# Kernel tuning notes

Measured on AMD Instinct MI355X. Metric: run time of the kernel, lower is better.

## Reference

```python
import jax, jax.numpy as jnp
import numpy as np

NUM_HEADS = 12
ALPHA = 4.0
EPS = 1e-6

def safe_pow(x, p):
    # relu(x)**p with grad-safe handling of x<=0 (avoids nan from log(0) in pow grads)
    xp = jnp.where(x > 0, x, 1.0)
    return jnp.where(x > 0, xp ** p, 0.0)

def setup_inputs() -> dict:
    key = jax.random.key(0)
    ks = jax.random.split(key, 9)
    B, N, C = 8, 4096, 768
    Hn, hd, ksz = NUM_HEADS, C // NUM_HEADS, 5
    return {
        "x": jax.random.normal(ks[0], (B, N, C), jnp.float32),
        "Wqg": jax.random.normal(ks[1], (C, 2 * C), jnp.float32) * 0.02,
        "Wkv": jax.random.normal(ks[2], (C, 2 * C), jnp.float32) * 0.02,
        "Wproj": jax.random.normal(ks[3], (C, C), jnp.float32) * 0.02,
        "bproj": jnp.zeros((C,), jnp.float32),
        "dwc_w": jax.random.normal(ks[4], (hd, 1, ksz, ksz), jnp.float32) * 0.05,
        "dwc_b": jnp.zeros((hd,), jnp.float32),
        "power_p": jax.random.normal(ks[5], (1, Hn, 1, hd), jnp.float32) * 0.01,
        "scale_p": jax.random.normal(ks[6], (1, 1, C), jnp.float32) * 0.01,
        "pos_enc": jax.random.normal(ks[7], (1, N, C), jnp.float32) * 0.01,
    }

def reference(x, Wqg, Wkv, Wproj, bproj, dwc_w, dwc_b, power_p, scale_p, pos_enc):
    B, N, C = x.shape
    Hn = NUM_HEADS
    hd = C // Hn
    # q/g projection: [B,N,2C] -> q = [...,0,:], g = [...,1,:]
    qg = (x @ Wqg).reshape(B, N, 2, C)
    q, g = qg[:, :, 0], qg[:, :, 1]
    # k/v projection (sr_ratio == 1)
    kvp = x @ Wkv
    k, v = kvp[..., :C], kvp[..., C:]
    k = k + pos_enc
    scale = jax.nn.softplus(scale_p)            # [1,1,C]
    power = 1.0 + ALPHA * jax.nn.sigmoid(power_p)  # [1,Hn,1,hd]
    q = q / scale
    k = k / scale
    # -> [B,Hn,N,hd]
    q = q.reshape(B, N, Hn, hd).transpose(0, 2, 1, 3)
    k = k.reshape(B, N, Hn, hd).transpose(0, 2, 1, 3)
    v = v.reshape(B, N, Hn, hd).transpose(0, 2, 1, 3)
    q_pos = safe_pow(q, power)
    q_neg = safe_pow(-q, power)
    k_pos = safe_pow(k, power)
    k_neg = safe_pow(-k, power)
    q_sim = jnp.concatenate([q_pos, q_neg], -1)  # [B,Hn,N,2hd]
    q_opp = jnp.concatenate([q_neg, q_pos], -1)
    k_cat = jnp.concatenate([k_pos, k_neg], -1)
    v1, v2 = jnp.split(v, 2, axis=-1)            # [B,Hn,N,hd/2]
    n = N
    inv_n = 1.0 / n
    k_mean = k_cat.mean(axis=2, keepdims=True)   # [B,Hn,1,2hd]
    z_sim = 1.0 / (jnp.einsum('bhnk,bhmk->bhnm', q_sim, k_mean) + EPS)  # [B,Hn,N,1]
    kv1 = jnp.einsum('bhnk,bhnv->bhkv', k_cat, v1) * inv_n
    x_sim = jnp.einsum('bhnk,bhkv->bhnv', q_sim, kv1) * z_sim
    z_opp = 1.0 / (jnp.einsum('bhnk,bhmk->bhnm', q_opp, k_mean) + EPS)
    kv2 = jnp.einsum('bhnk,bhnv->bhkv', k_cat, v2) * inv_n
    x_opp = jnp.einsum('bhnk,bhkv->bhnv', q_opp, kv2) * z_opp
    xa = jnp.concatenate([x_sim, x_opp], -1).transpose(0, 2, 1, 3).reshape(B, N, C)
    # depthwise-conv positional branch on v (head-major channel layout)
    Hs = int(np.sqrt(N))
    v_img = v.reshape(B * Hn, Hs, Hs, hd).transpose(0, 3, 1, 2)  # [B*Hn, hd, Hs, Hs]
    v_conv = jax.lax.conv_general_dilated(
        v_img, dwc_w, (1, 1), 'SAME', feature_group_count=hd,
        dimension_numbers=('NCHW', 'OIHW', 'NCHW')) + dwc_b[None, :, None, None]
    v_pos = v_conv.reshape(B, C, N).transpose(0, 2, 1)  # [B,N,C]
    out = (xa + v_pos) * g
    return out @ Wproj + bproj
```

## Files before the change

### kernel.cpp

```cpp
#include <hip/hip_runtime.h>


typedef _Float16 f16;
typedef __attribute__((ext_vector_type(4))) float f32x4;
typedef __attribute__((ext_vector_type(8))) _Float16 f16x8;
typedef __attribute__((ext_vector_type(4))) _Float16 f16x4;

__device__ __forceinline__ void mfma(f32x4& c, f16x8 a, f16x8 b) {
  c = __builtin_amdgcn_mfma_f32_16x16x32_f16(a, b, c, 0, 0, 0);
}

__device__ __forceinline__ void gload_lds16(const f16* g, f16* l) {
  __builtin_amdgcn_global_load_lds(
      (__attribute__((address_space(1))) void*)g,
      (__attribute__((address_space(3))) void*)l, 16, 0, 0);
}

__device__ __forceinline__ f16x8 relu8(f16x8 v) {
  f16x8 r;
#pragma unroll
  for (int u = 0; u < 8; ++u) r[u] = (v[u] > (f16)0) ? v[u] : (f16)0;
  return r;
}
__device__ __forceinline__ f16x8 nrelu8(f16x8 v) {
  f16x8 r;
#pragma unroll
  for (int u = 0; u < 8; ++u) r[u] = (v[u] < (f16)0) ? (f16)(-v[u]) : (f16)0;
  return r;
}

__global__ void prep_scalars_kernel(const float* __restrict__ scale_p,
                                    const float* __restrict__ power_p,
                                    float* __restrict__ iscale,
                                    float* __restrict__ powr) {
  int c = blockIdx.x * 256 + threadIdx.x;
  if (c < 768) {
    float sp = scale_p[c];
    float s = (sp > 20.f) ? sp : log1pf(__expf(sp));
    iscale[c] = 1.f / s;
    powr[c] = 1.f + 4.f / (1.f + __expf(-power_p[c]));
  }
}

__global__ __launch_bounds__(256) void cast_x_kernel(const float* __restrict__ x,
                                                     f16* __restrict__ xblk) {
  __shared__ f16 tile[128 * 72];
  const int kb = blockIdx.x, mt = blockIdx.y, t = threadIdx.x;
  const float* xp = x + (size_t)mt * 128 * 768 + kb * 64;
#pragma unroll
  for (int it = 0; it < 8; ++it) {
    int idx = it * 256 + t;
    int row = idx >> 4, kc4 = (idx & 15) * 4;
    f32x4 v = *(const f32x4*)(xp + (size_t)row * 768 + kc4);
    f16x4 h;
    h[0] = (f16)v[0]; h[1] = (f16)v[1]; h[2] = (f16)v[2]; h[3] = (f16)v[3];
    *(f16x4*)(tile + row * 72 + kc4) = h;
  }
  __syncthreads();
  f16* op = xblk + (size_t)mt * 98304 + kb * 8192;
#pragma unroll
  for (int it = 0; it < 4; ++it) {
    int c = it * 256 + t;
    int kchunk = c >> 7, m = c & 127;
    f16x4 lo = *(const f16x4*)(tile + m * 72 + kchunk * 8);
    f16x4 hi = *(const f16x4*)(tile + m * 72 + kchunk * 8 + 4);
    *(f16x4*)(op + c * 8) = lo;
    *(f16x4*)(op + c * 8 + 4) = hi;
  }
}

__global__ __launch_bounds__(256) void transpose_w_kernel(const float* __restrict__ W,
                                                          f16* __restrict__ outblk,
                                                          int Cc, int col_off) {
  __shared__ float tile[32][33];
  const int c0 = blockIdx.x * 32, r0 = blockIdx.y * 32, t = threadIdx.x;
#pragma unroll
  for (int it = 0; it < 4; ++it) {
    int rr = it * 8 + (t >> 5), cc = t & 31;
    tile[rr][cc] = W[(size_t)(r0 + rr) * Cc + c0 + cc];
  }
  __syncthreads();
  if (t < 128) {
    int cl = t >> 2, rb = t & 3;
    int cg = col_off + c0 + cl;
    int rg = r0 + rb * 8;
    f16x4 v0, v1;
#pragma unroll
    for (int u = 0; u < 4; ++u) v0[u] = (f16)tile[rb * 8 + u][cl];
#pragma unroll
    for (int u = 0; u < 4; ++u) v1[u] = (f16)tile[rb * 8 + 4 + u][cl];
    size_t base = (size_t)(cg >> 7) * 98304 + (size_t)(rg >> 3) * 1024 +
                  (size_t)(cg & 127) * 8;
    *(f16x4*)(outblk + base) = v0;
    *(f16x4*)(outblk + base + 4) = v1;
  }
}

template <int MODE>
__global__ __launch_bounds__(512, 4) void gemm_kernel(
    const f16* __restrict__ Ablk, const f16* __restrict__ Bblk,
    const float* __restrict__ powr, const float* __restrict__ iscale,
    const float* __restrict__ pos_enc, const float* __restrict__ bproj,
    f16* __restrict__ qpow, f16* __restrict__ gbuf, f16* __restrict__ kpow,
    f16* __restrict__ vt, float* __restrict__ outp) {
  constexpr int A_SZ = 4096;
  constexpr int STR  = 12288;
  __shared__ f16 smem[2 * STR];
  const int t = threadIdx.x;
  const int wid = t >> 6, lane = t & 63;
  const int c16 = lane & 15, q = lane >> 4;
  const int ntile = blockIdx.x, mtile = blockIdx.y;
  const int wm = wid >> 2, wn = wid & 3;
  const int bh2 = wn >> 1, bc = (wn & 1) * 64;
  const f16* Ap = Ablk + (size_t)mtile * 98304;
  const f16* Bp = Bblk + (size_t)ntile * 196608;

  auto STAGE = [&](int buf, int k0) {
    const size_t gk = (size_t)(k0 >> 3) * 1024;
    gload_lds16(Ap + gk + (size_t)t * 8, smem + buf * STR + wid * 512);
    gload_lds16(Bp + gk + (size_t)t * 8, smem + buf * STR + A_SZ + wid * 512);
    gload_lds16(Bp + 98304 + gk + (size_t)t * 8,
                smem + buf * STR + A_SZ + 4096 + wid * 512);
  };

  f32x4 acc[4][4];
#pragma unroll
  for (int i = 0; i < 4; ++i)
#pragma unroll
    for (int j = 0; j < 4; ++j) acc[i][j] = (f32x4){0.f, 0.f, 0.f, 0.f};

  STAGE(0, 0);
  asm volatile("s_waitcnt vmcnt(0)");
  __builtin_amdgcn_sched_barrier(0);
  __builtin_amdgcn_s_barrier();
  __builtin_amdgcn_sched_barrier(0);

  for (int j = 0; j < 24; ++j) {
    const int cur = j & 1;
    if (j < 23) STAGE(cur ^ 1, (j + 1) * 32);
    const f16* A_ = smem + cur * STR;
    const f16* B_ = smem + cur * STR + A_SZ + bh2 * 4096;
    f16x8 af[4], bf[4];
    const int kc = q * 1024;
#pragma unroll
    for (int mi = 0; mi < 4; ++mi)
      af[mi] = *(const f16x8*)(A_ + kc + (wm * 64 + mi * 16 + c16) * 8);
#pragma unroll
    for (int ni = 0; ni < 4; ++ni)
      bf[ni] = *(const f16x8*)(B_ + kc + (bc + ni * 16 + c16) * 8);
    asm volatile("s_waitcnt lgkmcnt(0)");
    __builtin_amdgcn_sched_barrier(0);
    __builtin_amdgcn_s_setprio(1);
#pragma unroll
    for (int mi = 0; mi < 4; ++mi)
#pragma unroll
      for (int ni = 0; ni < 4; ++ni) mfma(acc[mi][ni], af[mi], bf[ni]);
    __builtin_amdgcn_s_setprio(0);
    __builtin_amdgcn_sched_barrier(0);
    if (j < 23) asm volatile("s_waitcnt vmcnt(0)");
    __builtin_amdgcn_sched_barrier(0);
    __builtin_amdgcn_s_barrier();
    __builtin_amdgcn_sched_barrier(0);
  }

  if (MODE == 0) {
    const int sec = ntile / 3;
    const int csb = (ntile - sec * 3) * 256;
    const int b = mtile >> 5;
    const int nim0 = (mtile & 31) * 128;
#pragma unroll
    for (int mi = 0; mi < 4; ++mi) {
      const int nloc = nim0 + wm * 64 + mi * 16 + q * 4;
#pragma unroll
      for (int ni = 0; ni < 4; ++ni) {
        const int cs = csb + wn * 64 + ni * 16 + c16;
        const int h = cs >> 6, d = cs & 63;
        const int bh = b * 12 + h;
        if (sec == 0) {
          const float p = powr[cs], isc = iscale[cs];
          const size_t qb2 = (size_t)bh * 262144 + (size_t)(nloc >> 7) * 8192;
          const int dpo = (d >> 3) * 1024 + (d & 7);
#pragma unroll
          for (int r2 = 0; r2 < 4; ++r2) {
            float val = acc[mi][ni][r2] * isc;
            float av = fabsf(val);
            float e = (av > 0.f) ? exp2f(p * __log2f(av)) : 0.f;
            float s = (val > 0.f) ? e : ((val < 0.f) ? -e : 0.f);
            int mrow = (nloc + r2) & 127;
            qpow[qb2 + mrow * 8 + dpo] = (f16)s;
          }
        } else if (sec == 1) {
#pragma unroll
          for (int r2 = 0; r2 < 4; ++r2)
            gbuf[((size_t)bh * 4096 + nloc + r2) * 64 + d] = (f16)acc[mi][ni][r2];
        } else if (sec == 2) {
          const float p = powr[cs], isc = iscale[cs];
          f16x4 pk;
#pragma unroll
          for (int r2 = 0; r2 < 4; ++r2) {
            int n = nloc + r2;
            float val = (acc[mi][ni][r2] + pos_enc[(size_t)n * 768 + cs]) * isc;
            float av = fabsf(val);
            float e = (av > 0.f) ? exp2f(p * __log2f(av)) : 0.f;
            pk[r2] = (f16)((val > 0.f) ? e : ((val < 0.f) ? -e : 0.f));
          }
          const size_t kb2 =
              (size_t)bh * 262144 + (size_t)(nloc >> 3) * 512 + (nloc & 7);
          *(f16x4*)(kpow + kb2 + (size_t)d * 8) = pk;
        } else {
          f16x4 vv4;
#pragma unroll
          for (int r2 = 0; r2 < 4; ++r2) vv4[r2] = (f16)acc[mi][ni][r2];
          *(f16x4*)(vt + (size_t)(bh * 64 + d) * 4096 + nloc) = vv4;
        }
      }
    }
  } else {
#pragma unroll
    for (int mi = 0; mi < 4; ++mi) {
      const int tok0 = mtile * 128 + wm * 64 + mi * 16 + q * 4;
#pragma unroll
      for (int ni = 0; ni < 4; ++ni) {
        const int col = ntile * 256 + wn * 64 + ni * 16 + c16;
        const float bb = bproj[col];
#pragma unroll
        for (int r2 = 0; r2 < 4; ++r2)
          outp[(size_t)(tok0 + r2) * 768 + col] = acc[mi][ni][r2] + bb;
      }
    }
  }
}

__global__ __launch_bounds__(256) void kv_kernel(const f16* __restrict__ kpow,
                                                 const f16* __restrict__ vt,
                                                 float* __restrict__ kvp,
                                                 float* __restrict__ ksp) {
  __shared__ f16 Ks[8192];
  __shared__ f16 Vs[4096];
  __shared__ float rp[256], rn[256];
  const int bh = blockIdx.x, split = blockIdx.y, t = threadIdx.x;
  const int wave = t >> 6, lane = t & 63;
  const int c16 = lane & 15, q = lane >> 4;
  const f16* kb = kpow + (size_t)bh * 262144;
  const f16* vb = vt + (size_t)bh * 64 * 4096;
  f32x4 acc[4][2];
#pragma unroll
  for (int i = 0; i < 4; ++i)
#pragma unroll
    for (int j = 0; j < 2; ++j) acc[i][j] = (f32x4){0.f, 0.f, 0.f, 0.f};
  float sp = 0.f, sn = 0.f;

  const int n_beg = split * 1024, n_end = n_beg + 1024;
  for (int n0 = n_beg; n0 < n_end; n0 += 64) {
    f16x8 kr[2], vr[2];
#pragma unroll
    for (int r = 0; r < 2; ++r)
      kr[r] = *(const f16x8*)(kb + (size_t)n0 * 64 + (size_t)(r * 256 + t) * 8);
#pragma unroll
    for (int r = 0; r < 2; ++r) {
      int cc = r * 256 + t;
      int vv = cc >> 3, nc = cc & 7;
      vr[r] = *(const f16x8*)(vb + (size_t)vv * 4096 + n0 + nc * 8);
    }
#pragma unroll
    for (int r = 0; r < 2; ++r)
#pragma unroll
      for (int u = 0; u < 8; ++u) {
        float f = (float)kr[r][u];
        sp += (f > 0.f) ? f : 0.f;
        sn += (f < 0.f) ? -f : 0.f;
      }
    __syncthreads();
#pragma unroll
    for (int r = 0; r < 2; ++r) {
      int cp = r * 256 + t;
      int nch = cp >> 6, d = cp & 63;
      *(f16x8*)(Ks + (size_t)(nch * 1024 + d * 8)) = relu8(kr[r]);
      *(f16x8*)(Ks + (size_t)(nch * 1024 + (d + 64) * 8)) = nrelu8(kr[r]);
    }
#pragma unroll
    for (int r = 0; r < 2; ++r) {
      int cc = r * 256 + t;
      int vv = cc >> 3, nc = cc & 7;
      *(f16x8*)(Vs + (size_t)(nc * 64 + (vv ^ nc)) * 8) = vr[r];
    }
    __syncthreads();
#pragma unroll
    for (int s = 0; s < 2; ++s) {
      f16x8 af[4], bf2[2];
#pragma unroll
      for (int i = 0; i < 4; ++i) {
        int m = i * 16 + c16, nc2 = s * 4 + q;
        af[i] = *(const f16x8*)(Vs + (nc2 * 64 + (m ^ nc2)) * 8);
      }
#pragma unroll
      for (int j = 0; j < 2; ++j)
        bf2[j] = *(const f16x8*)(Ks + ((s * 4 + q) * 128 + wave * 32 + j * 16 + c16) * 8);
#pragma unroll
      for (int i = 0; i < 4; ++i)
#pragma unroll
        for (int j = 0; j < 2; ++j) mfma(acc[i][j], af[i], bf2[j]);
    }
    __syncthreads();
  }
  float* kvb = kvp + (size_t)(bh * 4 + split) * 8192;
#pragma unroll
  for (int i = 0; i < 4; ++i)
#pragma unroll
    for (int j = 0; j < 2; ++j) {
      int kk = wave * 32 + j * 16 + c16;
      int vv0 = i * 16 + q * 4;
#pragma unroll
      for (int r2 = 0; r2 < 4; ++r2)
        kvb[(size_t)(vv0 + r2) * 128 + kk] = acc[i][j][r2];
    }
  rp[t] = sp; rn[t] = sn;
  __syncthreads();
  if (t < 64) {
    float* ko = ksp + (size_t)(bh * 4 + split) * 128;
    ko[t] = rp[t] + rp[t + 64] + rp[t + 128] + rp[t + 192];
    ko[64 + t] = rn[t] + rn[t + 64] + rn[t + 128] + rn[t + 192];
  }
}

__global__ void bx_kernel(const float* __restrict__ kvp,
                          const float* __restrict__ ksp, f16* __restrict__ bxt) {
  const int bh = blockIdx.x, kk = threadIdx.x;
  const float inv_n = 1.f / 4096.f;
  const float* kv0 = kvp + (size_t)bh * 4 * 8192;
  const float* ks0 = ksp + (size_t)bh * 4 * 128;
  f16* ob = bxt + (size_t)bh * 80 * 128;
  for (int nn = 0; nn < 32; ++nn) {
    float v = kv0[nn * 128 + kk] + kv0[8192 + nn * 128 + kk] +
              kv0[16384 + nn * 128 + kk] + kv0[24576 + nn * 128 + kk];
    ob[nn * 128 + kk] = (f16)(v * inv_n);
  }
  const int kx = kk ^ 64;
  for (int nn = 32; nn < 64; ++nn) {
    float v = kv0[nn * 128 + kx] + kv0[8192 + nn * 128 + kx] +
              kv0[16384 + nn * 128 + kx] + kv0[24576 + nn * 128 + kx];
    ob[nn * 128 + kk] = (f16)(v * inv_n);
  }
  float s0 = ks0[kk] + ks0[128 + kk] + ks0[256 + kk] + ks0[384 + kk];
  ob[64 * 128 + kk] = (f16)(s0 * inv_n);
  float s1 = ks0[kx] + ks0[128 + kx] + ks0[256 + kx] + ks0[384 + kx];
  ob[65 * 128 + kk] = (f16)(s1 * inv_n);
  for (int nn = 66; nn < 80; ++nn) ob[nn * 128 + kk] = (f16)0.f;
}

__global__ __launch_bounds__(256) void conv_kernel(const f16* __restrict__ vt,
                                                   const float* __restrict__ w,
                                                   const float* __restrict__ bias,
                                                   f16* __restrict__ vpos) {
  __shared__ float img[68 * 69];
  const int blk = blockIdx.x;
  const int d = blk & 63, bh = blk >> 6;
  const f16* src = vt + (size_t)(bh * 64 + d) * 4096;
  for (int i = threadIdx.x; i < 68 * 68; i += 256) {
    int yy = i / 68, xx = i - yy * 68;
    int y = yy - 2, x = xx - 2;
    float val = 0.f;
    if (((unsigned)y < 64u) && ((unsigned)x < 64u)) val = (float)src[y * 64 + x];
    img[yy * 69 + xx] = val;
  }
  float wr[25];
#pragma unroll
  for (int k = 0; k < 25; ++k) wr[k] = w[d * 25 + k];
  const float bb = bias[d];
  __syncthreads();
  f16* dst = vpos + (size_t)(bh * 64 + d) * 4096;
  for (int g4 = threadIdx.x; g4 < 1024; g4 += 256) {
    int y = g4 >> 4, x4 = (g4 & 15) * 4;
    float o0 = bb, o1 = bb, o2 = bb, o3 = bb;
#pragma unroll
    for (int ky = 0; ky < 5; ++ky) {
      const float* row = img + (y + ky) * 69 + x4;
      float r[8];
#pragma unroll
      for (int u = 0; u < 8; ++u) r[u] = row[u];
#pragma unroll
      for (int kx = 0; kx < 5; ++kx) {
        float wv = wr[ky * 5 + kx];
        o0 += r[kx] * wv;
        o1 += r[kx + 1] * wv;
        o2 += r[kx + 2] * wv;
        o3 += r[kx + 3] * wv;
      }
    }
    f16x4 st;
    st[0] = (f16)o0; st[1] = (f16)o1; st[2] = (f16)o2; st[3] = (f16)o3;
    *(f16x4*)(dst + y * 64 + x4) = st;
  }
}

__global__ __launch_bounds__(256) void xa_kernel(
    const f16* __restrict__ qpow, const f16* __restrict__ bxt,
    const f16* __restrict__ vpos, const f16* __restrict__ gbuf,
    f16* __restrict__ pre) {
  __shared__ f16 Qs[16384];
  __shared__ f16 Ps[64 * 134];
  __shared__ float zs[256];
  const int nb = blockIdx.x, bh = blockIdx.y;
  const int b = bh / 12, h = bh % 12;
  const int t = threadIdx.x;
  const int wave = t >> 6, lane = t & 63;
  const int c16 = lane & 15, q = lane >> 4;
  const f16* qb = qpow + (size_t)bh * 262144 + (size_t)nb * 8192;
  f16x8 qr[4];
#pragma unroll
  for (int r = 0; r < 4; ++r)
    qr[r] = *(const f16x8*)(qb + (size_t)(r * 256 + t) * 8);
#pragma unroll
  for (int r = 0; r < 4; ++r) {
    int c = r * 256 + t;
    int dch = c >> 7, row = c & 127;
    *(f16x8*)(Qs + (size_t)(dch * 1024 + row * 8)) = relu8(qr[r]);
    *(f16x8*)(Qs + (size_t)((dch + 8) * 1024 + row * 8)) = nrelu8(qr[r]);
  }
  {
    const f16* vpb = vpos + (size_t)bh * 262144 + (size_t)nb * 128;
#pragma unroll
    for (int it = 0; it < 4; ++it) {
      int idx = it * 256 + t;
      int col = idx >> 4, nc = idx & 15;
      f16x8 v = *(const f16x8*)(vpb + (size_t)col * 4096 + nc * 8);
      *(f16x8*)(Ps + col * 134 + nc * 8) = v;
    }
  }
  __syncthreads();
  f32x4 acc[2][5];
#pragma unroll
  for (int i = 0; i < 2; ++i)
#pragma unroll
    for (int j = 0; j < 5; ++j) acc[i][j] = (f32x4){0.f, 0.f, 0.f, 0.f};
  const f16* bx = bxt + (size_t)bh * 80 * 128;
#pragma unroll
  for (int s = 0; s < 4; ++s) {
    f16x8 af[2], bf5[5];
#pragma unroll
    for (int i = 0; i < 2; ++i)
      af[i] = *(const f16x8*)(Qs + ((s * 4 + q) * 1024 + (wave * 32 + i * 16 + c16) * 8));
#pragma unroll
    for (int j = 0; j < 5; ++j)
      bf5[j] = *(const f16x8*)(bx + (size_t)(j * 16 + c16) * 128 + s * 32 + q * 8);
#pragma unroll
    for (int i = 0; i < 2; ++i)
#pragma unroll
      for (int j = 0; j < 5; ++j) mfma(acc[i][j], af[i], bf5[j]);
  }
  if (c16 < 2) {
#pragma unroll
    for (int i = 0; i < 2; ++i) {
      int mloc = wave * 32 + i * 16 + q * 4;
#pragma unroll
      for (int r2 = 0; r2 < 4; ++r2) zs[(mloc + r2) * 2 + c16] = acc[i][4][r2];
    }
  }
  __syncthreads();
#pragma unroll
  for (int i = 0; i < 2; ++i) {
    const int mbase = wave * 32 + i * 16 + q * 4;
#pragma unroll
    for (int j = 0; j < 4; ++j) {
      const int col = j * 16 + c16;
      const int cch = h * 64 + col;
      const int zsel = col >> 5;
#pragma unroll
      for (int r2 = 0; r2 < 4; ++r2) {
        const int mloc = mbase + r2;
        const int n = nb * 128 + mloc;
        const float den = zs[mloc * 2 + zsel];
        const float xav = acc[i][j][r2] / (den + 1e-6f);
        const float vp = (float)Ps[col * 134 + mloc];
        const float gg = (float)gbuf[((size_t)bh * 4096 + n) * 64 + col];
        const int tok = b * 4096 + n;
        pre[(size_t)(tok >> 7) * 98304 + (size_t)(cch >> 3) * 1024 +
            (tok & 127) * 8 + (cch & 7)] = (f16)((xav + vp) * gg);
      }
    }
  }
}

extern "C" void kernel_launch(void* const* d_in, const int* in_sizes, int n_in,
                              void* d_out, int out_size, void* d_ws, size_t ws_size,
                              hipStream_t stream) {
  const float* x       = (const float*)d_in[0];
  const float* Wqg     = (const float*)d_in[1];
  const float* Wkv     = (const float*)d_in[2];
  const float* Wproj   = (const float*)d_in[3];
  const float* bproj   = (const float*)d_in[4];
  const float* dwc_w   = (const float*)d_in[5];
  const float* dwc_b   = (const float*)d_in[6];
  const float* power_p = (const float*)d_in[7];
  const float* scale_p = (const float*)d_in[8];
  const float* pos_enc = (const float*)d_in[9];
  float* outp = (float*)d_out;

  char* ws = (char*)d_ws;
  constexpr size_t o_qpow = 0;
  constexpr size_t o_kpow = 50331648;
  constexpr size_t o_vt   = 100663296;
  constexpr size_t o_gbuf = 150994944;
  constexpr size_t o_xblk = 201326592;
  constexpr size_t o_wta  = 251658240;
  constexpr size_t o_wtp  = 256376832;
  constexpr size_t o_isc  = 257556480;
  constexpr size_t o_pwr  = 257560576;
  constexpr size_t o_bxt  = 257564672;

  f16*   qpow = (f16*)(ws + o_qpow);
  f16*   kpow = (f16*)(ws + o_kpow);
  f16*   vt   = (f16*)(ws + o_vt);
  f16*   gbuf = (f16*)(ws + o_gbuf);
  f16*   xblk = (f16*)(ws + o_xblk);
  f16*   wta  = (f16*)(ws + o_wta);
  f16*   wtp  = (f16*)(ws + o_wtp);
  float* isc  = (float*)(ws + o_isc);
  float* pwr  = (float*)(ws + o_pwr);
  f16*   bxt  = (f16*)(ws + o_bxt);
  float* kvp  = (float*)(ws + o_xblk);
  float* ksp  = (float*)(ws + o_xblk + 12582912);
  f16*   vpos = kpow;
  f16*   pre  = xblk;

  prep_scalars_kernel<<<dim3(3), 256, 0, stream>>>(scale_p, power_p, isc, pwr);
  cast_x_kernel<<<dim3(12, 256), 256, 0, stream>>>(x, xblk);
  transpose_w_kernel<<<dim3(48, 24), 256, 0, stream>>>(Wqg, wta, 1536, 0);
  transpose_w_kernel<<<dim3(48, 24), 256, 0, stream>>>(Wkv, wta, 1536, 1536);
  transpose_w_kernel<<<dim3(24, 24), 256, 0, stream>>>(Wproj, wtp, 768, 0);
  gemm_kernel<0><<<dim3(12, 256), 512, 0, stream>>>(
      xblk, wta, pwr, isc, pos_enc, nullptr, qpow, gbuf, kpow, vt, nullptr);
  kv_kernel<<<dim3(96, 4), 256, 0, stream>>>(kpow, vt, kvp, ksp);
  bx_kernel<<<96, 128, 0, stream>>>(kvp, ksp, bxt);
  conv_kernel<<<6144, 256, 0, stream>>>(vt, dwc_w, dwc_b, vpos);
  xa_kernel<<<dim3(32, 96), 256, 0, stream>>>(qpow, bxt, vpos, gbuf, pre);
  gemm_kernel<1><<<dim3(3, 256), 512, 0, stream>>>(
      pre, wtp, nullptr, nullptr, nullptr, bproj, nullptr, nullptr, nullptr,
      nullptr, outp);
}
```

Measured before the change: 617.0 us.

## Triple-buffer GEMM staging, block gbuf layout, vectorize conv and xa global I/O

The GEMM main loop moves from two to three LDS stages and prefetches two k-steps ahead, waiting only on the older stage's loads. The g projection is now written in the same blocked token/channel layout as the pre-projection buffer. The xa kernel can then load g with coalesced 16-byte reads, stage its output tile in LDS and write it back with vector stores instead of scattered 2-byte writes. The conv kernel loads its image rows as 4-wide f16 vectors and zeroes the halo columns separately. The extra GEMM stage raises LDS use per block, which may lower occupancy at the 4-blocks-per-CU launch bound.

```diff
diff --git a/kernel.cpp b/kernel.cpp
--- a/kernel.cpp
+++ b/kernel.cpp
@@ -105,7 +105,7 @@
     f16* __restrict__ vt, float* __restrict__ outp) {
   constexpr int A_SZ = 4096;
   constexpr int STR  = 12288;
-  __shared__ f16 smem[2 * STR];
+  __shared__ f16 smem[3 * STR];
   const int t = threadIdx.x;
   const int wid = t >> 6, lane = t & 63;
   const int c16 = lane & 15, q = lane >> 4;
@@ -130,14 +130,15 @@
     for (int j = 0; j < 4; ++j) acc[i][j] = (f32x4){0.f, 0.f, 0.f, 0.f};
 
   STAGE(0, 0);
-  asm volatile("s_waitcnt vmcnt(0)");
+  STAGE(1, 32);
+  asm volatile("s_waitcnt vmcnt(3)");
   __builtin_amdgcn_sched_barrier(0);
   __builtin_amdgcn_s_barrier();
   __builtin_amdgcn_sched_barrier(0);
 
+  int cur = 0, nx2 = 2;
   for (int j = 0; j < 24; ++j) {
-    const int cur = j & 1;
-    if (j < 23) STAGE(cur ^ 1, (j + 1) * 32);
+    if (j < 22) STAGE(nx2, (j + 2) * 32);
     const f16* A_ = smem + cur * STR;
     const f16* B_ = smem + cur * STR + A_SZ + bh2 * 4096;
     f16x8 af[4], bf[4];
@@ -157,10 +158,13 @@
       for (int ni = 0; ni < 4; ++ni) mfma(acc[mi][ni], af[mi], bf[ni]);
     __builtin_amdgcn_s_setprio(0);
     __builtin_amdgcn_sched_barrier(0);
-    if (j < 23) asm volatile("s_waitcnt vmcnt(0)");
+    if (j < 22)       asm volatile("s_waitcnt vmcnt(3)");
+    else if (j == 22) asm volatile("s_waitcnt vmcnt(0)");
     __builtin_amdgcn_sched_barrier(0);
     __builtin_amdgcn_s_barrier();
     __builtin_amdgcn_sched_barrier(0);
+    cur = (cur == 2) ? 0 : cur + 1;
+    nx2 = (nx2 == 2) ? 0 : nx2 + 1;
   }
 
   if (MODE == 0) {
@@ -191,8 +195,11 @@
           }
         } else if (sec == 1) {
 #pragma unroll
-          for (int r2 = 0; r2 < 4; ++r2)
-            gbuf[((size_t)bh * 4096 + nloc + r2) * 64 + d] = (f16)acc[mi][ni][r2];
+          for (int r2 = 0; r2 < 4; ++r2) {
+            const int tok = b * 4096 + nloc + r2;
+            gbuf[(size_t)(tok >> 7) * 98304 + (size_t)(cs >> 3) * 1024 +
+                 (tok & 127) * 8 + (cs & 7)] = (f16)acc[mi][ni][r2];
+          }
         } else if (sec == 2) {
           const float p = powr[cs], isc = iscale[cs];
           f16x4 pk;
@@ -356,12 +363,21 @@
   const int blk = blockIdx.x;
   const int d = blk & 63, bh = blk >> 6;
   const f16* src = vt + (size_t)(bh * 64 + d) * 4096;
-  for (int i = threadIdx.x; i < 68 * 68; i += 256) {
-    int yy = i / 68, xx = i - yy * 68;
-    int y = yy - 2, x = xx - 2;
-    float val = 0.f;
-    if (((unsigned)y < 64u) && ((unsigned)x < 64u)) val = (float)src[y * 64 + x];
-    img[yy * 69 + xx] = val;
+  for (int i = threadIdx.x; i < 68 * 16; i += 256) {
+    int yy = i >> 4, g4 = i & 15;
+    int y = yy - 2;
+    float v0 = 0.f, v1 = 0.f, v2 = 0.f, v3 = 0.f;
+    if ((unsigned)y < 64u) {
+      f16x4 v = *(const f16x4*)(src + y * 64 + g4 * 4);
+      v0 = (float)v[0]; v1 = (float)v[1]; v2 = (float)v[2]; v3 = (float)v[3];
+    }
+    float* row = img + yy * 69 + 2 + g4 * 4;
+    row[0] = v0; row[1] = v1; row[2] = v2; row[3] = v3;
+  }
+  for (int i = threadIdx.x; i < 68 * 4; i += 256) {
+    int yy = i >> 2, c = i & 3;
+    int xx = (c < 2) ? c : 64 + c;
+    img[yy * 69 + xx] = 0.f;
   }
   float wr[25];
 #pragma unroll
@@ -406,10 +422,14 @@
   const int wave = t >> 6, lane = t & 63;
   const int c16 = lane & 15, q = lane >> 4;
   const f16* qb = qpow + (size_t)bh * 262144 + (size_t)nb * 8192;
-  f16x8 qr[4];
+  const size_t gp2 = (size_t)(b * 32 + nb) * 98304 + (size_t)(h * 8) * 1024;
+  f16x8 qr[4], gr[4];
 #pragma unroll
   for (int r = 0; r < 4; ++r)
     qr[r] = *(const f16x8*)(qb + (size_t)(r * 256 + t) * 8);
+#pragma unroll
+  for (int r = 0; r < 4; ++r)
+    gr[r] = *(const f16x8*)(gbuf + gp2 + (size_t)(r * 256 + t) * 8);
 #pragma unroll
   for (int r = 0; r < 4; ++r) {
     int c = r * 256 + t;
@@ -457,28 +477,36 @@
     }
   }
   __syncthreads();
+  f16* Gs = Qs;
+  f16* Os = Qs + 8192;
+#pragma unroll
+  for (int r = 0; r < 4; ++r)
+    *(f16x8*)(Gs + (size_t)(r * 256 + t) * 8) = gr[r];
+  __syncthreads();
 #pragma unroll
   for (int i = 0; i < 2; ++i) {
     const int mbase = wave * 32 + i * 16 + q * 4;
 #pragma unroll
     for (int j = 0; j < 4; ++j) {
       const int col = j * 16 + c16;
-      const int cch = h * 64 + col;
       const int zsel = col >> 5;
+      const int gidx = (col >> 3) * 1024 + (col & 7);
 #pragma unroll
       for (int r2 = 0; r2 < 4; ++r2) {
         const int mloc = mbase + r2;
-        const int n = nb * 128 + mloc;
         const float den = zs[mloc * 2 + zsel];
         const float xav = acc[i][j][r2] / (den + 1e-6f);
         const float vp = (float)Ps[col * 134 + mloc];
-        const float gg = (float)gbuf[((size_t)bh * 4096 + n) * 64 + col];
-        const int tok = b * 4096 + n;
-        pre[(size_t)(tok >> 7) * 98304 + (size_t)(cch >> 3) * 1024 +
-            (tok & 127) * 8 + (cch & 7)] = (f16)((xav + vp) * gg);
+        const float gg = (float)Gs[gidx + mloc * 8];
+        Os[gidx + mloc * 8] = (f16)((xav + vp) * gg);
       }
     }
   }
+  __syncthreads();
+#pragma unroll
+  for (int r = 0; r < 4; ++r)
+    *(f16x8*)(pre + gp2 + (size_t)(r * 256 + t) * 8) =
+        *(const f16x8*)(Os + (size_t)(r * 256 + t) * 8);
 }
 
 extern "C" void kernel_launch(void* const* d_in, const int* in_sizes, int n_in,
```

New measurement: 590.5 us. -4.3%, faster.
